# Performance work log

Hardware: AMD Instinct MI355X
Metric: run time of the kernel (lower is better)

Reference implementation:

```python
import jax, jax.numpy as jnp
import numpy as np

OUT = 7   # output_size
SR = 2    # sampling_ratio
SCALES = (0.25, 0.125, 0.0625, 0.03125)  # inferred from feat sizes vs 800x800 image
K_MIN, LVL0, S0, EPS = 2, 4.0, 224.0, 1e-6


def _bilinear_gather(feat, b, y, x):
    """Legacy (aligned=False) bilinear sampling. feat [B,C,H,W]; b,y,x same shape S.
    Returns [*S, C]."""
    B, C, H, W = feat.shape
    valid = (y >= -1.0) & (y <= H) & (x >= -1.0) & (x <= W)
    y = jnp.maximum(y, 0.0)
    x = jnp.maximum(x, 0.0)
    yl = y.astype(jnp.int32)
    xl = x.astype(jnp.int32)
    ycond = yl >= H - 1
    yl = jnp.where(ycond, H - 1, yl)
    yh = jnp.where(ycond, H - 1, yl + 1)
    y = jnp.where(ycond, yl.astype(y.dtype), y)
    xcond = xl >= W - 1
    xl = jnp.where(xcond, W - 1, xl)
    xh = jnp.where(xcond, W - 1, xl + 1)
    x = jnp.where(xcond, xl.astype(x.dtype), x)
    ly = y - yl
    lx = x - xl
    hy = 1.0 - ly
    hx = 1.0 - lx
    def g(yy, xx):
        return feat[b, :, yy, xx]  # advanced indexing -> [*S, C]
    val = ((hy * hx)[..., None] * g(yl, xl)
           + (hy * lx)[..., None] * g(yl, xh)
           + (ly * hx)[..., None] * g(yh, xl)
           + (ly * lx)[..., None] * g(yh, xh))
    return jnp.where(valid[..., None], val, 0.0)


def _roi_align(feat, bidx, boxes, scale):
    """RoIAlign (aligned=False). feat [B,C,H,W], bidx [R] int, boxes [R,4] image coords.
    Returns [R,C,OUT,OUT]."""
    x1 = boxes[:, 0] * scale
    y1 = boxes[:, 1] * scale
    x2 = boxes[:, 2] * scale
    y2 = boxes[:, 3] * scale
    roi_w = jnp.maximum(x2 - x1, 1.0)
    roi_h = jnp.maximum(y2 - y1, 1.0)
    bin_h = roi_h / OUT
    bin_w = roi_w / OUT
    off = (jnp.arange(SR, dtype=feat.dtype) + 0.5) / SR      # [SR]
    ph = jnp.arange(OUT, dtype=feat.dtype)                   # [OUT]
    grid = ph[None, :, None] + off[None, None, :]            # [1,OUT,SR]
    ys = y1[:, None, None] + grid * bin_h[:, None, None]     # [R,OUT,SR]
    xs = x1[:, None, None] + grid * bin_w[:, None, None]     # [R,OUT,SR]
    Y = ys[:, :, None, :, None]                              # [R,OUT,1,SR,1]
    X = xs[:, None, :, None, :]                              # [R,1,OUT,1,SR]
    Yb, Xb = jnp.broadcast_arrays(Y, X)                      # [R,OUT,OUT,SR,SR]
    b = jnp.broadcast_to(bidx[:, None, None, None, None], Yb.shape)
    val = _bilinear_gather(feat, b, Yb, Xb)                  # [R,OUT,OUT,SR,SR,C]
    pooled = val.mean(axis=(3, 4))                           # [R,OUT,OUT,C]
    return jnp.transpose(pooled, (0, 3, 1, 2))               # [R,C,OUT,OUT]


def _levels(boxes_flat):
    """LevelMapper.run: FPN level index (0-based) per RoI."""
    area = (boxes_flat[:, 2] - boxes_flat[:, 0]) * (boxes_flat[:, 3] - boxes_flat[:, 1])
    s = jnp.sqrt(area)
    lvl = jnp.floor(LVL0 + jnp.log2(s / S0 + EPS))
    return jnp.clip(lvl, K_MIN, K_MIN + 3).astype(jnp.int32) - K_MIN


def setup_inputs() -> dict:
    key = jax.random.key(0)
    ks = jax.random.split(key, 6)
    sizes = [200, 100, 50, 25]
    inp = {f"feat{i}": jax.random.normal(ks[i], (2, 256, s, s), dtype=jnp.float32)
           for i, s in enumerate(sizes)}
    xy = jax.random.uniform(ks[4], (2, 256, 2), dtype=jnp.float32) * 500.0
    wh = jax.random.uniform(ks[5], (2, 256, 2), dtype=jnp.float32) * 400.0 + 8.0
    inp["boxes"] = jnp.concatenate([xy, xy + wh], axis=-1)  # (x1,y1,x2,y2) in [0,908)
    return inp


def reference(feat0, feat1, feat2, feat3, boxes):
    feats = [feat0, feat1, feat2, feat3]
    B, N, _ = boxes.shape
    bf = boxes.reshape(B * N, 4)
    bidx = jnp.repeat(jnp.arange(B, dtype=jnp.int32), N)  # convert_to_roi_format ids
    lv = _levels(bf)
    C = feats[0].shape[1]
    out = jnp.zeros((B * N, C, OUT, OUT), dtype=feats[0].dtype)
    for level, (f, sc) in enumerate(zip(feats, SCALES)):
        r = _roi_align(f, bidx, bf, sc)
        out = jnp.where((lv == level)[:, None, None, None], r, out)
    return out
```

## Files before the change

kernel.cpp:

```cpp
#include <hip/hip_runtime.h>

#define OUT 7
#define NCH 256
#define NROI 512
#define NS 14
#define NT 28
#define CCH 16
#define W9 9
#define WPC 253
#define TPR (NCH * OUT * OUT)

__device__ __forceinline__ float rfl_f(float v) {
    return __int_as_float(__builtin_amdgcn_readfirstlane(__float_as_int(v)));
}

__device__ __forceinline__ unsigned short f2bf_rne(float f) {
    unsigned int u = __float_as_uint(f);
    u += 0x7FFFu + ((u >> 16) & 1u);
    return (unsigned short)(u >> 16);
}

__global__ __launch_bounds__(256, 4) void roi_align_tap16_kernel(
        const float* __restrict__ f0, const float* __restrict__ f1,
        const float* __restrict__ f2, const float* __restrict__ f3,
        const float* __restrict__ boxes, float* __restrict__ out) {
    __shared__ unsigned short sm[NT * WPC * 2];
    __shared__ int   rowIdx[NT];
    __shared__ int   colIdx[NT];
    __shared__ float lyS[NS], vyS[NS], lxS[NS], vxS[NS];

    int g    = blockIdx.x;
    int xcd  = g & 7;
    int slot = g >> 3;
    int rr   = slot >> 4;
    int q    = slot & 15;
    int r    = rr * 8 + xcd;
    int tid  = (int)threadIdx.x;

    float bx1 = rfl_f(boxes[r * 4 + 0]);
    float by1 = rfl_f(boxes[r * 4 + 1]);
    float bx2 = rfl_f(boxes[r * 4 + 2]);
    float by2 = rfl_f(boxes[r * 4 + 3]);

    float area = (bx2 - bx1) * (by2 - by1);
    float s    = sqrtf(area);
    float lvl  = floorf(4.0f + log2f(s * (1.0f / 224.0f) + 1e-6f));
    lvl        = fminf(fmaxf(lvl, 2.0f), 5.0f);
    int level  = __builtin_amdgcn_readfirstlane((int)lvl - 2);

    const float* f; int H; float scale;
    switch (level) {
        case 0:  f = f0; H = 200; scale = 0.25f;    break;
        case 1:  f = f1; H = 100; scale = 0.125f;   break;
        case 2:  f = f2; H = 50;  scale = 0.0625f;  break;
        default: f = f3; H = 25;  scale = 0.03125f; break;
    }
    float Hf = (float)H;

    float x1 = bx1 * scale, y1 = by1 * scale;
    float roi_w = fmaxf(bx2 * scale - x1, 1.0f);
    float roi_h = fmaxf(by2 * scale - y1, 1.0f);
    float bin_w = roi_w * (1.0f / OUT);
    float bin_h = roi_h * (1.0f / OUT);

    if (tid < NS) {
        int ph = tid >> 1, iy = tid & 1;
        float y = y1 + ((float)ph + (iy ? 0.75f : 0.25f)) * bin_h;
        float v = (y >= -1.0f && y <= Hf) ? 0.5f : 0.0f;
        y = fmaxf(y, 0.0f);
        int yl = (int)y, yh;
        float ly;
        if (yl >= H - 1) { yl = H - 1; yh = H - 1; ly = 0.0f; }
        else             { yh = yl + 1; ly = y - (float)yl; }
        lyS[tid] = ly; vyS[tid] = v;
        rowIdx[2 * tid]     = yl;
        rowIdx[2 * tid + 1] = yh;
    } else if (tid >= 32 && tid < 32 + NS) {
        int t = tid - 32;
        int pw = t >> 1, ix = t & 1;
        float x = x1 + ((float)pw + (ix ? 0.75f : 0.25f)) * bin_w;
        float v = (x >= -1.0f && x <= Hf) ? 0.5f : 0.0f;
        x = fmaxf(x, 0.0f);
        int xl = (int)x, xh;
        float lx;
        if (xl >= H - 1) { xl = H - 1; xh = H - 1; lx = 0.0f; }
        else             { xh = xl + 1; lx = x - (float)xl; }
        lxS[t] = lx; vxS[t] = v;
        colIdx[2 * t]     = xl;
        colIdx[2 * t + 1] = xh;
    }
    __syncthreads();

    int bidx = r >> 8;
    size_t HH = (size_t)(H * H);
    const float* plane = f + (size_t)(bidx * NCH + q * CCH) * HH;

    int lane = tid & 63;
    int wave = tid >> 6;
    int  j   = (lane < 28) ? lane : ((lane < 56) ? lane - 28 : lane - 56);
    int  cg  = (lane >= 28 && lane < 56) ? 1 : 0;
    bool act = (lane < 56);
    int  col = colIdx[j];

#pragma unroll
    for (int t = 0; t < 7; ++t) {
        int rs = wave * 7 + t;
        size_t rbase = (size_t)rowIdx[rs] * (size_t)H + (size_t)col;
        float v[8];
#pragma unroll
        for (int cc = 0; cc < 8; ++cc)
            v[cc] = plane[(size_t)(cg * 8 + cc) * HH + rbase];
        unsigned short* dstp = sm + (j * WPC + rs * W9) * 2 + cg * 8;
#pragma unroll
        for (int cc = 0; cc < 8; ++cc)
            if (act) dstp[cc] = f2bf_rne(v[cc]);
    }
    __syncthreads();

    const unsigned int* smw = (const unsigned int*)sm;
    float accx[2], accy[2];
#pragma unroll
    for (int i = 0; i < 2; ++i) { accx[i] = 0.0f; accy[i] = 0.0f; }

#pragma unroll
    for (int i = 0; i < 2; ++i) {
        int o = tid + 256 * i;
        if (o < 392) {
            int cp = o & 7, px = o >> 3;
            int ph = px / 7, pw = px - ph * 7;
            float ax = 0.0f, ay = 0.0f;
#pragma unroll
            for (int iy = 0; iy < 2; ++iy) {
                int sy = ph * 2 + iy;
                float ly = lyS[sy], hy = 1.0f - ly;
                float vy = vyS[sy];
                int r0 = (2 * sy) * W9 + cp;
                int r1 = r0 + W9;
#pragma unroll
                for (int ix = 0; ix < 2; ++ix) {
                    int sx = pw * 2 + ix;
                    float lx = lxS[sx], hx = 1.0f - lx;
                    float m  = vy * vxS[sx];
                    int c0 = (2 * sx) * WPC;
                    int c1 = c0 + WPC;
                    unsigned int u00 = smw[c0 + r0];
                    unsigned int u01 = smw[c1 + r0];
                    unsigned int u10 = smw[c0 + r1];
                    unsigned int u11 = smw[c1 + r1];
                    float w00 = hy * hx * m, w01 = hy * lx * m;
                    float w10 = ly * hx * m, w11 = ly * lx * m;
                    ax = fmaf(w00, __uint_as_float(u00 << 16), ax);
                    ay = fmaf(w00, __uint_as_float(u00 & 0xFFFF0000u), ay);
                    ax = fmaf(w01, __uint_as_float(u01 << 16), ax);
                    ay = fmaf(w01, __uint_as_float(u01 & 0xFFFF0000u), ay);
                    ax = fmaf(w10, __uint_as_float(u10 << 16), ax);
                    ay = fmaf(w10, __uint_as_float(u10 & 0xFFFF0000u), ay);
                    ax = fmaf(w11, __uint_as_float(u11 << 16), ax);
                    ay = fmaf(w11, __uint_as_float(u11 & 0xFFFF0000u), ay);
                }
            }
            accx[i] = ax; accy[i] = ay;
        }
    }
    __syncthreads();

    float* smf = (float*)sm;
#pragma unroll
    for (int i = 0; i < 2; ++i) {
        int o = tid + 256 * i;
        if (o < 392) {
            int cp = o & 7, px = o >> 3;
            smf[(cp * 2 + 0) * 49 + px] = accx[i];
            smf[(cp * 2 + 1) * 49 + px] = accy[i];
        }
    }
    __syncthreads();

    float* dst = out + (size_t)r * TPR + (size_t)q * (CCH * 49);
    for (int e = tid; e < CCH * 49; e += 256) dst[e] = smf[e];
}

extern "C" void kernel_launch(void* const* d_in, const int* in_sizes, int n_in,
                              void* d_out, int out_size, void* d_ws, size_t ws_size,
                              hipStream_t stream) {
    const float* f0    = (const float*)d_in[0];
    const float* f1    = (const float*)d_in[1];
    const float* f2    = (const float*)d_in[2];
    const float* f3    = (const float*)d_in[3];
    const float* boxes = (const float*)d_in[4];
    float* out         = (float*)d_out;

    roi_align_tap16_kernel<<<NROI * 16, 256, 0, stream>>>(f0, f1, f2, f3, boxes, out);
}
```

Before: 181.4 us.

## Gather tap column pairs with float2 loads and packed bf16 convert

The gather phase is restructured so each lane loads both adjacent columns (xl, xl+1) with one float2 load per channel, handling the clamped edge with a select. All 28 loads per lane are issued up front, which raises memory-level parallelism. Conversion to bf16 now uses the hardware v_cvt_pk_bf16_f32 instruction with packed 32-bit LDS stores in place of scalar 16-bit ones. The final output copy is vectorised to float4. Register pressure goes up from holding 56 loaded floats per lane, and the float2 loads may be unaligned.

```diff
diff --git a/kernel.cpp b/kernel.cpp
--- a/kernel.cpp
+++ b/kernel.cpp
@@ -14,19 +14,26 @@
     return __int_as_float(__builtin_amdgcn_readfirstlane(__float_as_int(v)));
 }
 
-__device__ __forceinline__ unsigned short f2bf_rne(float f) {
-    unsigned int u = __float_as_uint(f);
-    u += 0x7FFFu + ((u >> 16) & 1u);
-    return (unsigned short)(u >> 16);
+__device__ __forceinline__ float2 ld2(const float* p) {
+    float2 r;
+    __builtin_memcpy(&r, p, sizeof(float2));
+    return r;
+}
+
+__device__ __forceinline__ unsigned int cvt_pk_bf16(float lo, float hi) {
+    unsigned int r;
+    asm("v_cvt_pk_bf16_f32 %0, %1, %2" : "=v"(r) : "v"(lo), "v"(hi));
+    return r;
 }
 
 __global__ __launch_bounds__(256, 4) void roi_align_tap16_kernel(
         const float* __restrict__ f0, const float* __restrict__ f1,
         const float* __restrict__ f2, const float* __restrict__ f3,
         const float* __restrict__ boxes, float* __restrict__ out) {
-    __shared__ unsigned short sm[NT * WPC * 2];
+    __shared__ __align__(16) unsigned short sm[NT * WPC * 2];
     __shared__ int   rowIdx[NT];
-    __shared__ int   colIdx[NT];
+    __shared__ int   c0S[NS];
+    __shared__ int   selS[NS];
     __shared__ float lyS[NS], vyS[NS], lxS[NS], vxS[NS];
 
     int g    = blockIdx.x;
@@ -81,13 +88,12 @@
         float x = x1 + ((float)pw + (ix ? 0.75f : 0.25f)) * bin_w;
         float v = (x >= -1.0f && x <= Hf) ? 0.5f : 0.0f;
         x = fmaxf(x, 0.0f);
-        int xl = (int)x, xh;
-        float lx;
-        if (xl >= H - 1) { xl = H - 1; xh = H - 1; lx = 0.0f; }
-        else             { xh = xl + 1; lx = x - (float)xl; }
+        int xl = (int)x;
+        float lx; int c0, sel;
+        if (xl >= H - 1) { c0 = H - 2; sel = 1; lx = 0.0f; }
+        else             { c0 = xl;    sel = 0; lx = x - (float)xl; }
         lxS[t] = lx; vxS[t] = v;
-        colIdx[2 * t]     = xl;
-        colIdx[2 * t + 1] = xh;
+        c0S[t] = c0; selS[t] = sel;
     }
     __syncthreads();
 
@@ -97,23 +103,46 @@
 
     int lane = tid & 63;
     int wave = tid >> 6;
-    int  j   = (lane < 28) ? lane : ((lane < 56) ? lane - 28 : lane - 56);
-    int  cg  = (lane >= 28 && lane < 56) ? 1 : 0;
-    bool act = (lane < 56);
-    int  col = colIdx[j];
-
+    int cq   = lane / 14;  if (cq > 3) cq = 3;
+    int sp   = lane - cq * 14;  if (sp > 13) sp = 13;
+    bool act = lane < 56;
+    int  c0  = c0S[sp];
+    bool sel = selS[sp] != 0;
+
+    const float* base = plane + (size_t)(cq * 4) * HH;
+
+    int roff[7];
+#pragma unroll
+    for (int t = 0; t < 7; ++t)
+        roff[t] = rowIdx[wave * 7 + t] * H + c0;
+
+    float2 v[7][4];
+#pragma unroll
+    for (int t = 0; t < 7; ++t)
+#pragma unroll
+        for (int cc = 0; cc < 4; ++cc)
+            v[t][cc] = ld2(base + (size_t)cc * HH + (size_t)roff[t]);
+
+    unsigned int* smw_w = (unsigned int*)sm;
+    int wbase = (2 * sp) * WPC + 2 * cq;
 #pragma unroll
     for (int t = 0; t < 7; ++t) {
         int rs = wave * 7 + t;
-        size_t rbase = (size_t)rowIdx[rs] * (size_t)H + (size_t)col;
-        float v[8];
-#pragma unroll
-        for (int cc = 0; cc < 8; ++cc)
-            v[cc] = plane[(size_t)(cg * 8 + cc) * HH + rbase];
-        unsigned short* dstp = sm + (j * WPC + rs * W9) * 2 + cg * 8;
-#pragma unroll
-        for (int cc = 0; cc < 8; ++cc)
-            if (act) dstp[cc] = f2bf_rne(v[cc]);
+        float l0 = sel ? v[t][0].y : v[t][0].x;
+        float l1 = sel ? v[t][1].y : v[t][1].x;
+        float l2 = sel ? v[t][2].y : v[t][2].x;
+        float l3 = sel ? v[t][3].y : v[t][3].x;
+        unsigned int lo01 = cvt_pk_bf16(l0, l1);
+        unsigned int lo23 = cvt_pk_bf16(l2, l3);
+        unsigned int hi01 = cvt_pk_bf16(v[t][0].y, v[t][1].y);
+        unsigned int hi23 = cvt_pk_bf16(v[t][2].y, v[t][3].y);
+        if (act) {
+            unsigned int* d0 = smw_w + wbase + rs * W9;
+            d0[0]       = lo01;
+            d0[1]       = lo23;
+            d0[WPC]     = hi01;
+            d0[WPC + 1] = hi23;
+        }
     }
     __syncthreads();
 
@@ -141,12 +170,12 @@
                     int sx = pw * 2 + ix;
                     float lx = lxS[sx], hx = 1.0f - lx;
                     float m  = vy * vxS[sx];
-                    int c0 = (2 * sx) * WPC;
-                    int c1 = c0 + WPC;
-                    unsigned int u00 = smw[c0 + r0];
-                    unsigned int u01 = smw[c1 + r0];
-                    unsigned int u10 = smw[c0 + r1];
-                    unsigned int u11 = smw[c1 + r1];
+                    int c0i = (2 * sx) * WPC;
+                    int c1i = c0i + WPC;
+                    unsigned int u00 = smw[c0i + r0];
+                    unsigned int u01 = smw[c1i + r0];
+                    unsigned int u10 = smw[c0i + r1];
+                    unsigned int u11 = smw[c1i + r1];
                     float w00 = hy * hx * m, w01 = hy * lx * m;
                     float w10 = ly * hx * m, w11 = ly * lx * m;
                     ax = fmaf(w00, __uint_as_float(u00 << 16), ax);
@@ -177,7 +206,8 @@
     __syncthreads();
 
     float* dst = out + (size_t)r * TPR + (size_t)q * (CCH * 49);
-    for (int e = tid; e < CCH * 49; e += 256) dst[e] = smf[e];
+    if (tid < 196)
+        ((float4*)dst)[tid] = ((const float4*)smf)[tid];
 }
 
 extern "C" void kernel_launch(void* const* d_in, const int* in_sizes, int n_in,
```

After: 178.9 us. Within noise of the previous version (-1.4%).

## Stage contiguous ROI footprint rows into LDS instead of per-tap gathers

Applied to the files above, without the earlier changes.

Each block now computes the bounding rectangle of all sampled rows and columns for its ROI. It loads that rectangle row by row with coalesced lane-contiguous reads, instead of gathering the 28x28 tap positions individually. Loads are software-pipelined four rows deep, and channels are packed in pairs to bf16 with the hardware pack instruction. The output store is widened to float4. The aim is to cut scattered global accesses and redundant tap reads. In exchange, the LDS staging is a fixed 901-word plane per channel pair, and thin, elongated boxes could exceed it.

```diff
diff --git a/kernel.cpp b/kernel.cpp
--- a/kernel.cpp
+++ b/kernel.cpp
@@ -4,37 +4,45 @@
 #define NCH 256
 #define NROI 512
 #define NS 14
-#define NT 28
 #define CCH 16
-#define W9 9
-#define WPC 253
+#define PLANE 901
 #define TPR (NCH * OUT * OUT)
 
 __device__ __forceinline__ float rfl_f(float v) {
     return __int_as_float(__builtin_amdgcn_readfirstlane(__float_as_int(v)));
 }
 
-__device__ __forceinline__ unsigned short f2bf_rne(float f) {
-    unsigned int u = __float_as_uint(f);
-    u += 0x7FFFu + ((u >> 16) & 1u);
-    return (unsigned short)(u >> 16);
-}
-
-__global__ __launch_bounds__(256, 4) void roi_align_tap16_kernel(
+__device__ __forceinline__ unsigned int cvt_pk_bf16(float lo, float hi) {
+    unsigned int r;
+    asm("v_cvt_pk_bf16_f32 %0, %1, %2" : "=v"(r) : "v"(lo), "v"(hi));
+    return r;
+}
+
+__device__ __forceinline__ void tap1d(float start, float bin, int sidx, int H,
+                                      int& lo, int& hi, float& fr, float& vv) {
+    int p = sidx >> 1, half = sidx & 1;
+    float c = start + ((float)p + (half ? 0.75f : 0.25f)) * bin;
+    vv = (c >= -1.0f && c <= (float)H) ? 0.5f : 0.0f;
+    c = fmaxf(c, 0.0f);
+    int l = (int)c;
+    if (l >= H - 1) { lo = H - 1; hi = H - 1; fr = 0.0f; }
+    else            { lo = l;     hi = l + 1; fr = c - (float)l; }
+}
+
+__global__ __launch_bounds__(256, 4) void roi_align_fp_kernel(
         const float* __restrict__ f0, const float* __restrict__ f1,
         const float* __restrict__ f2, const float* __restrict__ f3,
         const float* __restrict__ boxes, float* __restrict__ out) {
-    __shared__ unsigned short sm[NT * WPC * 2];
-    __shared__ int   rowIdx[NT];
-    __shared__ int   colIdx[NT];
+    __shared__ __align__(16) unsigned int sm32[8 * PLANE];
     __shared__ float lyS[NS], vyS[NS], lxS[NS], vxS[NS];
+    __shared__ int rowLrel[NS], rowHrel[NS], colLrel[NS], colHrel[NS];
 
     int g    = blockIdx.x;
     int xcd  = g & 7;
     int slot = g >> 3;
-    int rr   = slot >> 4;
+    int rr_  = slot >> 4;
     int q    = slot & 15;
-    int r    = rr * 8 + xcd;
+    int r    = rr_ * 8 + xcd;
     int tid  = (int)threadIdx.x;
 
     float bx1 = rfl_f(boxes[r * 4 + 0]);
@@ -55,7 +63,6 @@
         case 2:  f = f2; H = 50;  scale = 0.0625f;  break;
         default: f = f3; H = 25;  scale = 0.03125f; break;
     }
-    float Hf = (float)H;
 
     float x1 = bx1 * scale, y1 = by1 * scale;
     float roi_w = fmaxf(bx2 * scale - x1, 1.0f);
@@ -63,61 +70,76 @@
     float bin_w = roi_w * (1.0f / OUT);
     float bin_h = roi_h * (1.0f / OUT);
 
+    int lo0, hi0, lo13, hi13; float frT, vvT;
+    tap1d(y1, bin_h, 0,  H, lo0, hi0, frT, vvT);
+    tap1d(y1, bin_h, 13, H, lo13, hi13, frT, vvT);
+    int rowMin = __builtin_amdgcn_readfirstlane(lo0);
+    int rowMax = __builtin_amdgcn_readfirstlane(hi13);
+    tap1d(x1, bin_w, 0,  H, lo0, hi0, frT, vvT);
+    tap1d(x1, bin_w, 13, H, lo13, hi13, frT, vvT);
+    int colMin = __builtin_amdgcn_readfirstlane(lo0);
+    int colMax = __builtin_amdgcn_readfirstlane(hi13);
+    int Ht = rowMax - rowMin + 1;
+    int Wd = colMax - colMin + 1;
+
     if (tid < NS) {
-        int ph = tid >> 1, iy = tid & 1;
-        float y = y1 + ((float)ph + (iy ? 0.75f : 0.25f)) * bin_h;
-        float v = (y >= -1.0f && y <= Hf) ? 0.5f : 0.0f;
-        y = fmaxf(y, 0.0f);
-        int yl = (int)y, yh;
-        float ly;
-        if (yl >= H - 1) { yl = H - 1; yh = H - 1; ly = 0.0f; }
-        else             { yh = yl + 1; ly = y - (float)yl; }
-        lyS[tid] = ly; vyS[tid] = v;
-        rowIdx[2 * tid]     = yl;
-        rowIdx[2 * tid + 1] = yh;
+        int lo, hi; float fr, vv;
+        tap1d(y1, bin_h, tid, H, lo, hi, fr, vv);
+        lyS[tid] = fr; vyS[tid] = vv;
+        rowLrel[tid] = lo - rowMin; rowHrel[tid] = hi - rowMin;
     } else if (tid >= 32 && tid < 32 + NS) {
         int t = tid - 32;
-        int pw = t >> 1, ix = t & 1;
-        float x = x1 + ((float)pw + (ix ? 0.75f : 0.25f)) * bin_w;
-        float v = (x >= -1.0f && x <= Hf) ? 0.5f : 0.0f;
-        x = fmaxf(x, 0.0f);
-        int xl = (int)x, xh;
-        float lx;
-        if (xl >= H - 1) { xl = H - 1; xh = H - 1; lx = 0.0f; }
-        else             { xh = xl + 1; lx = x - (float)xl; }
-        lxS[t] = lx; vxS[t] = v;
-        colIdx[2 * t]     = xl;
-        colIdx[2 * t + 1] = xh;
-    }
-    __syncthreads();
+        int lo, hi; float fr, vv;
+        tap1d(x1, bin_w, t, H, lo, hi, fr, vv);
+        lxS[t] = fr; vxS[t] = vv;
+        colLrel[t] = lo - colMin; colHrel[t] = hi - colMin;
+    }
 
     int bidx = r >> 8;
     size_t HH = (size_t)(H * H);
-    const float* plane = f + (size_t)(bidx * NCH + q * CCH) * HH;
-
     int lane = tid & 63;
-    int wave = tid >> 6;
-    int  j   = (lane < 28) ? lane : ((lane < 56) ? lane - 28 : lane - 56);
-    int  cg  = (lane >= 28 && lane < 56) ? 1 : 0;
-    bool act = (lane < 56);
-    int  col = colIdx[j];
-
-#pragma unroll
-    for (int t = 0; t < 7; ++t) {
-        int rs = wave * 7 + t;
-        size_t rbase = (size_t)rowIdx[rs] * (size_t)H + (size_t)col;
-        float v[8];
-#pragma unroll
-        for (int cc = 0; cc < 8; ++cc)
-            v[cc] = plane[(size_t)(cg * 8 + cc) * HH + rbase];
-        unsigned short* dstp = sm + (j * WPC + rs * W9) * 2 + cg * 8;
-#pragma unroll
-        for (int cc = 0; cc < 8; ++cc)
-            if (act) dstp[cc] = f2bf_rne(v[cc]);
+    int wv   = __builtin_amdgcn_readfirstlane(tid >> 6);
+
+    const float* pw0 = f + ((size_t)(bidx * NCH + q * CCH + 4 * wv)) * HH
+                         + (size_t)(rowMin * H + colMin);
+    size_t HH1 = HH, HH2 = 2 * HH, HH3 = 3 * HH;
+    int wb0 = (2 * wv) * PLANE;
+    int wb1 = wb0 + PLANE;
+
+    bool TWO = (Wd > 64);
+    int  cA  = (lane < Wd) ? lane : (Wd - 1);
+    int  cB  = TWO ? ((lane + 64 < Wd) ? lane + 64 : Wd - 1) : 0;
+    bool wA  = (lane < Wd);
+    bool wB  = TWO && (lane + 64 < Wd);
+
+#define DECLS(s) float A##s, B##s, C##s, D##s, E##s = 0, F##s = 0, G##s = 0, I##s = 0;
+    DECLS(0) DECLS(1) DECLS(2) DECLS(3)
+
+#define STG_ISSUE(s, rv) { \
+        int rr = (rv) < Ht ? (rv) : (Ht - 1); \
+        const float* p = pw0 + (size_t)(rr * H); \
+        A##s = p[cA]; B##s = p[HH1 + cA]; C##s = p[HH2 + cA]; D##s = p[HH3 + cA]; \
+        if (TWO) { E##s = p[cB]; F##s = p[HH1 + cB]; G##s = p[HH2 + cB]; I##s = p[HH3 + cB]; } }
+
+#define STG_CONSUME(s, rv) { \
+        if ((rv) < Ht) { \
+            int wb = (rv) * Wd + lane; \
+            if (wA) { \
+                sm32[wb0 + wb] = cvt_pk_bf16(A##s, B##s); \
+                sm32[wb1 + wb] = cvt_pk_bf16(C##s, D##s); } \
+            if (wB) { \
+                sm32[wb0 + wb + 64] = cvt_pk_bf16(E##s, F##s); \
+                sm32[wb1 + wb + 64] = cvt_pk_bf16(G##s, I##s); } } }
+
+    STG_ISSUE(0, 0) STG_ISSUE(1, 1) STG_ISSUE(2, 2) STG_ISSUE(3, 3)
+    for (int rw = 0; rw < Ht; rw += 4) {
+        STG_CONSUME(0, rw)     STG_ISSUE(0, rw + 4)
+        STG_CONSUME(1, rw + 1) STG_ISSUE(1, rw + 5)
+        STG_CONSUME(2, rw + 2) STG_ISSUE(2, rw + 6)
+        STG_CONSUME(3, rw + 3) STG_ISSUE(3, rw + 7)
     }
     __syncthreads();
 
-    const unsigned int* smw = (const unsigned int*)sm;
     float accx[2], accy[2];
 #pragma unroll
     for (int i = 0; i < 2; ++i) { accx[i] = 0.0f; accy[i] = 0.0f; }
@@ -128,25 +150,25 @@
         if (o < 392) {
             int cp = o & 7, px = o >> 3;
             int ph = px / 7, pw = px - ph * 7;
+            int cpP = cp * PLANE;
             float ax = 0.0f, ay = 0.0f;
 #pragma unroll
             for (int iy = 0; iy < 2; ++iy) {
                 int sy = ph * 2 + iy;
                 float ly = lyS[sy], hy = 1.0f - ly;
                 float vy = vyS[sy];
-                int r0 = (2 * sy) * W9 + cp;
-                int r1 = r0 + W9;
+                int rL = cpP + rowLrel[sy] * Wd;
+                int rH = cpP + rowHrel[sy] * Wd;
 #pragma unroll
                 for (int ix = 0; ix < 2; ++ix) {
                     int sx = pw * 2 + ix;
                     float lx = lxS[sx], hx = 1.0f - lx;
                     float m  = vy * vxS[sx];
-                    int c0 = (2 * sx) * WPC;
-                    int c1 = c0 + WPC;
-                    unsigned int u00 = smw[c0 + r0];
-                    unsigned int u01 = smw[c1 + r0];
-                    unsigned int u10 = smw[c0 + r1];
-                    unsigned int u11 = smw[c1 + r1];
+                    int cL = colLrel[sx], cH = colHrel[sx];
+                    unsigned int u00 = sm32[rL + cL];
+                    unsigned int u01 = sm32[rL + cH];
+                    unsigned int u10 = sm32[rH + cL];
+                    unsigned int u11 = sm32[rH + cH];
                     float w00 = hy * hx * m, w01 = hy * lx * m;
                     float w10 = ly * hx * m, w11 = ly * lx * m;
                     ax = fmaf(w00, __uint_as_float(u00 << 16), ax);
@@ -164,7 +186,7 @@
     }
     __syncthreads();
 
-    float* smf = (float*)sm;
+    float* smf = (float*)sm32;
 #pragma unroll
     for (int i = 0; i < 2; ++i) {
         int o = tid + 256 * i;
@@ -177,7 +199,8 @@
     __syncthreads();
 
     float* dst = out + (size_t)r * TPR + (size_t)q * (CCH * 49);
-    for (int e = tid; e < CCH * 49; e += 256) dst[e] = smf[e];
+    if (tid < 196)
+        ((float4*)dst)[tid] = ((const float4*)smf)[tid];
 }
 
 extern "C" void kernel_launch(void* const* d_in, const int* in_sizes, int n_in,
@@ -190,5 +213,5 @@
     const float* boxes = (const float*)d_in[4];
     float* out         = (float*)d_out;
 
-    roi_align_tap16_kernel<<<NROI * 16, 256, 0, stream>>>(f0, f1, f2, f3, boxes, out);
-}
+    roi_align_fp_kernel<<<NROI * 16, 256, 0, stream>>>(f0, f1, f2, f3, boxes, out);
+}
```

New measurement: 194.1 us. 1.07x slower.
